# Performance work log

Hardware: AMD Instinct MI355X
Metric: run time of the kernel (lower is better)

## Reference

```python
import jax, jax.numpy as jnp
import numpy as np

SHIFT, REDUCE = 1, 2
B, L, E, H = 128, 64, 512, 512
T = 2 * L - 1  # valid binary-parse transition sequence length


def _make_transitions(rng):
    # Random *valid* shift-reduce sequences: L shifts, L-1 reduces, stack ends at 1.
    trans = np.zeros((B, T), dtype=np.int32)
    for b in range(B):
        stack, buf = 0, L
        for t in range(T):
            ops_left = T - t
            can_shift = buf > 0 and stack < ops_left
            can_reduce = stack >= 2
            if can_shift and can_reduce:
                act = SHIFT if rng.random() < 0.5 else REDUCE
            elif can_shift:
                act = SHIFT
            else:
                act = REDUCE
            if act == SHIFT:
                buf -= 1; stack += 1
            else:
                stack -= 1
            trans[b, t] = act
    return trans


def setup_inputs() -> dict:
    key = jax.random.key(0)
    k1, k2, k3, k4 = jax.random.split(key, 4)
    sentence = jax.random.normal(k1, (B, L, E), dtype=jnp.float32)
    transitions = jnp.asarray(_make_transitions(np.random.default_rng(0)))
    W_word = jax.random.normal(k2, (E, 2 * H), dtype=jnp.float32) / np.sqrt(E).astype(np.float32)
    b_word = jnp.zeros((2 * H,), dtype=jnp.float32)
    W_left = jax.random.normal(k3, (H, 5 * H), dtype=jnp.float32) / np.sqrt(H).astype(np.float32)
    W_right = jax.random.normal(k4, (H, 5 * H), dtype=jnp.float32) / np.sqrt(H).astype(np.float32)
    b_reduce = jnp.zeros((5 * H,), dtype=jnp.float32)
    return {"sentence": sentence, "transitions": transitions, "W_word": W_word,
            "b_word": b_word, "W_left": W_left, "W_right": W_right, "b_reduce": b_reduce}


def reference(sentence, transitions, W_word, b_word, W_left, W_right, b_reduce):
    Bx, Lx, _ = sentence.shape
    Hx = W_left.shape[0]
    Tx = transitions.shape[1]
    # word projection (no_batch_norm=True, dropout=0 in this config)
    out = sentence @ W_word + b_word                      # [B, L, 2H]
    h_buf, c_buf = jnp.split(out, 2, axis=2)              # buffers, popped front-to-back
    rows = jnp.arange(Bx)
    ops_left_seq = jnp.arange(Tx, 0, -1, dtype=jnp.int32)
    init = (jnp.zeros((Bx, Lx, Hx), out.dtype),           # stack h
            jnp.zeros((Bx, Lx, Hx), out.dtype),           # stack c
            jnp.zeros((Bx,), jnp.int32),                  # stack ptr
            jnp.zeros((Bx,), jnp.int32))                  # buffer ptr

    def step(carry, xs):
        sh, sc, sp, bp = carry
        act, ops = xs
        act = jnp.where(sp > ops, REDUCE, act)            # forced reduce (discrete stack)
        is_red = act == REDUCE
        is_shf = act == SHIFT
        r_idx = jnp.clip(sp - 1, 0, Lx - 1)
        l_idx = jnp.clip(sp - 2, 0, Lx - 1)
        hl, cl = sh[rows, l_idx], sc[rows, l_idx]
        hr, cr = sh[rows, r_idx], sc[rows, r_idx]
        # TreeLSTM Reduce cell
        gates = hl @ W_left + hr @ W_right + b_reduce     # [B, 5H]
        g, i, f1, f2, o = jnp.split(gates, 5, axis=1)
        c_red = jnp.tanh(g) * jax.nn.sigmoid(i) + jax.nn.sigmoid(f1) * cl + jax.nn.sigmoid(f2) * cr
        h_red = jax.nn.sigmoid(o) * jnp.tanh(c_red)
        b_idx = jnp.clip(bp, 0, Lx - 1)
        h_shf, c_shf = h_buf[rows, b_idx], c_buf[rows, b_idx]
        w_idx = jnp.where(is_red, l_idx, jnp.clip(sp, 0, Lx - 1))
        h_cur, c_cur = sh[rows, w_idx], sc[rows, w_idx]
        m_red, m_shf = is_red[:, None], is_shf[:, None]
        wh = jnp.where(m_red, h_red, jnp.where(m_shf, h_shf, h_cur))
        wc = jnp.where(m_red, c_red, jnp.where(m_shf, c_shf, c_cur))
        sh = sh.at[rows, w_idx].set(wh)
        sc = sc.at[rows, w_idx].set(wc)
        sp = sp + is_shf.astype(jnp.int32) - is_red.astype(jnp.int32)
        bp = bp + is_shf.astype(jnp.int32)
        return (sh, sc, sp, bp), None

    (sh, sc, sp, bp), _ = jax.lax.scan(step, init, (transitions.T, ops_left_seq))
    return sh[rows, jnp.clip(sp - 1, 0, Lx - 1)]          # [B, H] top of each stack
```

## Files before the change

### kernel.cpp

```cpp
#include <hip/hip_runtime.h>
#include <hip/hip_bf16.h>


#define Bn 128
#define Ln 64
#define En 512
#define Hn 512
#define Tn 127
#define LEAF_ROWS (Bn*Ln)
#define NODE_ROWS (Bn*(Ln-1))
#define TOT_ROWS (LEAF_ROWS+NODE_ROWS)
#define NLVL 64
#define NXCD 8
#define CAPX 512
#define NBLK 512
#define FPAD 16
#define MAXRANK 96
#define SPIN_CAP (1<<22)
#define GATE_STRIDE (512*1024)
#define WLDS_BYTES 65536
#define PART_BYTES (4*2*16*20*4)
#define DYN_BYTES (WLDS_BYTES + PART_BYTES)

#define OFF_CENSUS 0
#define OFF_RANK   (OFF_CENSUS + NXCD*FPAD)
#define OFF_SFLAG  (OFF_RANK + NBLK*FPAD)
#define OFF_SGEN   (OFF_SFLAG + NBLK*FPAD)
#define OFF_FX     (OFF_SGEN + FPAD)
#define OFF_GX     (OFF_FX + NXCD*MAXRANK*FPAD)
#define BAR_INTS   (OFF_GX + NXCD*FPAD)

typedef __attribute__((ext_vector_type(8))) short bf16x8;
typedef __attribute__((ext_vector_type(4))) float f32x4;

static __device__ __forceinline__ float bf2f(unsigned short u){
  unsigned v = ((unsigned)u) << 16;
  float f; __builtin_memcpy(&f, &v, 4); return f;
}
static __device__ __forceinline__ unsigned short f2bf(float f){
  unsigned u; __builtin_memcpy(&u, &f, 4);
  u = u + 0x7FFFu + ((u >> 16) & 1u);
  return (unsigned short)(u >> 16);
}
static __device__ __forceinline__ float sigm(float x){
  return 1.0f / (1.0f + __expf(-x));
}
static __device__ __forceinline__ float tanh_fast(float x){
  x = fminf(fmaxf(x, -15.0f), 15.0f);
  float t = __expf(2.0f * x);
  return (t - 1.0f) / (t + 1.0f);
}
static __device__ __forceinline__ int xcc_id(){
  unsigned v;
  asm volatile("s_getreg_b32 %0, hwreg(HW_REG_XCC_ID)" : "=s"(v));
  return (int)(v & 7);
}

static __device__ __forceinline__ void xcd_barrier(int* bar, int x, int rank, int nx, int epoch){
  __syncthreads();
  int* fx = bar + OFF_FX + x * MAXRANK * FPAD;
  int* gx = bar + OFF_GX + x * FPAD;
  int nxl = min(nx, MAXRANK);
  if (rank == 0){
    for (int i = threadIdx.x + 1; i < nxl; i += 256){
      int c = 0;
      while (__hip_atomic_load(&fx[i * FPAD], __ATOMIC_RELAXED, __HIP_MEMORY_SCOPE_AGENT) < epoch && c < SPIN_CAP){
        __builtin_amdgcn_s_sleep(1); ++c;
      }
    }
    __syncthreads();
    if (threadIdx.x == 0)
      __hip_atomic_store(gx, epoch, __ATOMIC_RELAXED, __HIP_MEMORY_SCOPE_AGENT);
  } else {
    if (threadIdx.x == 0){
      __hip_atomic_store(&fx[rank * FPAD], epoch, __ATOMIC_RELAXED, __HIP_MEMORY_SCOPE_AGENT);
      int c = 0;
      while (__hip_atomic_load(gx, __ATOMIC_RELAXED, __HIP_MEMORY_SCOPE_AGENT) < epoch && c < SPIN_CAP){
        __builtin_amdgcn_s_sleep(2); ++c;
      }
    }
    __syncthreads();
  }
  asm volatile("" ::: "memory");
}


__global__ void cvt_vec4(const float4* __restrict__ x, ushort4* __restrict__ y, int n4){
  int i = blockIdx.x * 256 + threadIdx.x;
  if (i < n4){
    float4 v = x[i];
    ushort4 o;
    o.x = f2bf(v.x); o.y = f2bf(v.y); o.z = f2bf(v.z); o.w = f2bf(v.w);
    y[i] = o;
  }
}

__global__ void transpose_cvt(const float* __restrict__ src, unsigned short* __restrict__ dstT,
                              int CS, int DS, int koff){
  __shared__ float tile[32][33];
  int c0 = blockIdx.x * 32, r0 = blockIdx.y * 32;
  int tx = threadIdx.x, ty = threadIdx.y;
  for (int i = ty; i < 32; i += 8) tile[i][tx] = src[(size_t)(r0 + i) * CS + c0 + tx];
  __syncthreads();
  for (int i = ty; i < 32; i += 8)
    dstT[(size_t)(c0 + i) * DS + koff + r0 + tx] = f2bf(tile[tx][i]);
}

__global__ void precompute_ctrl(const int* __restrict__ trans,
                                int* __restrict__ srcL, int* __restrict__ srcR,
                                int* __restrict__ dstv, int* __restrict__ cnt,
                                int* __restrict__ outsrc, int* __restrict__ bar){
  __shared__ int stk[Bn][Ln + 1];
  __shared__ int scnt[NXCD * NLVL];
  __shared__ int smaxl[NXCD];
  int b = threadIdx.x;
  for (int i = b; i < NXCD * NLVL; i += 128) scnt[i] = 0;
  if (b < NXCD) smaxl[b] = 0;
  for (int i = b; i < BAR_INTS; i += 128) bar[i] = 0;
  __syncthreads();
  int x = b & 7;
  int sp = 0, bp = 0, nodecnt = 0;
  int act_next = trans[b * Tn];
  for (int t = 0; t < Tn; t++){
    int act = act_next;
    if (t + 1 < Tn) act_next = trans[b * Tn + t + 1];
    int ops = Tn - t;
    if (sp > ops) act = 2;
    if (act == 2){
      int R = stk[b][sp - 1], L = stk[b][sp - 2];
      int lvl = max(R >> 20, L >> 20) + 1;
      int slot = atomicAdd(&scnt[x * NLVL + lvl], 1);
      int base = (x * NLVL + lvl) * CAPX + slot;
      srcL[base] = (L & 0xFFFFF) * Hn;
      srcR[base] = (R & 0xFFFFF) * Hn;
      int noderow = LEAF_ROWS + b * (Ln - 1) + nodecnt;
      dstv[base] = noderow * Hn;
      stk[b][sp - 2] = noderow | (lvl << 20);
      sp -= 1; nodecnt++;
    } else {
      stk[b][sp] = b * Ln + min(bp, Ln - 1);
      sp += 1; bp += 1;
    }
  }
  int root = stk[b][max(sp - 1, 0)];
  outsrc[b] = (root & 0xFFFFF) * Hn;
  atomicMax(&smaxl[x], root >> 20);
  __syncthreads();
  for (int i = b; i < NXCD * NLVL; i += 128) cnt[i] = scnt[i];
  if (b < NXCD) cnt[NXCD * NLVL + b] = smaxl[b];
}

__global__ __launch_bounds__(256) void word_gemm(
    const unsigned short* __restrict__ SB, const unsigned short* __restrict__ WwT,
    const float* __restrict__ b_word,
    unsigned short* __restrict__ HB, float* __restrict__ CF){
  int mt = blockIdx.x;
  int nt = blockIdx.y;
  int tid = threadIdx.x, w = tid >> 6, lane = tid & 63;
  int wm = w >> 1, wn = w & 1;
  int rc = lane & 15, lg = lane >> 4;
  const unsigned short* ap0 = SB + (size_t)(mt * 64 + wm * 32 + rc) * En + lg * 8;
  const unsigned short* ap1 = ap0 + (size_t)16 * En;
  const unsigned short* bp0 = WwT + (size_t)(nt * 128 + wn * 64 + rc) * En + lg * 8;
  f32x4 acc[2][4];
  #pragma unroll
  for (int h = 0; h < 2; h++)
    #pragma unroll
    for (int nb = 0; nb < 4; nb++) acc[h][nb] = (f32x4){0.f,0.f,0.f,0.f};

  bf16x8 a0c = *(const bf16x8*)ap0;
  bf16x8 a1c = *(const bf16x8*)ap1;
  bf16x8 bc[4];
  #pragma unroll
  for (int nb = 0; nb < 4; nb++) bc[nb] = *(const bf16x8*)(bp0 + (size_t)nb * 16 * En);

  #pragma unroll
  for (int j = 0; j < 16; ++j){
    bf16x8 a0n, a1n, bn[4];
    if (j < 15){
      int kn = (j + 1) * 32;
      a0n = *(const bf16x8*)(ap0 + kn);
      a1n = *(const bf16x8*)(ap1 + kn);
      #pragma unroll
      for (int nb = 0; nb < 4; nb++)
        bn[nb] = *(const bf16x8*)(bp0 + (size_t)nb * 16 * En + kn);
    }
    #pragma unroll
    for (int nb = 0; nb < 4; nb++){
      acc[0][nb] = __builtin_amdgcn_mfma_f32_16x16x32_bf16(a0c, bc[nb], acc[0][nb], 0, 0, 0);
      acc[1][nb] = __builtin_amdgcn_mfma_f32_16x16x32_bf16(a1c, bc[nb], acc[1][nb], 0, 0, 0);
    }
    a0c = a0n; a1c = a1n;
    #pragma unroll
    for (int nb = 0; nb < 4; nb++) bc[nb] = bn[nb];
  }
  #pragma unroll
  for (int nb = 0; nb < 4; nb++){
    int col = nt * 128 + wn * 64 + nb * 16 + rc;
    float bw = b_word[col];
    #pragma unroll
    for (int h = 0; h < 2; h++){
      #pragma unroll
      for (int q = 0; q < 4; q++){
        int row = mt * 64 + wm * 32 + h * 16 + lg * 4 + q;
        float v = acc[h][nb][q] + bw;
        if (col < Hn) HB[(size_t)row * Hn + col] = f2bf(v);
        else          CF[(size_t)row * Hn + (col - Hn)] = v;
      }
    }
  }
}

template<bool LDSB>
static __device__ __forceinline__ void tile64(
    int u0, int t, int nr, const int* __restrict__ sL, const int* __restrict__ sR,
    const int* __restrict__ dl,
    unsigned short* __restrict__ HB, float* __restrict__ CF,
    const unsigned short* __restrict__ WT, const float* __restrict__ b_red,
    const unsigned short* __restrict__ wlds, int rc, int lg)
{
  int base = t * 64;
  int offL[4], offR[4];
  #pragma unroll
  for (int m = 0; m < 4; m++){
    int i = min(base + m * 16 + rc, nr - 1);
    offL[m] = sL[i]; offR[m] = sR[i];
  }
  f32x4 acc[5][4];
  #pragma unroll
  for (int g = 0; g < 5; g++)
    #pragma unroll
    for (int m = 0; m < 4; m++) acc[g][m] = (f32x4){0.f,0.f,0.f,0.f};

  int bswz = (rc & 7) << 3;
  const unsigned short* gb = WT + (size_t)(u0 + rc) * 1024 + lg * 8;

  bf16x8 a_cur[4], b_cur[3];
  #pragma unroll
  for (int m = 0; m < 4; m++) a_cur[m] = *(const bf16x8*)(HB + offL[m] + lg * 8);
  #pragma unroll
  for (int g = 0; g < 3; g++)
    b_cur[g] = *(const bf16x8*)(gb + (size_t)(g + 2) * GATE_STRIDE);

  #pragma unroll 4
  for (int j = 0; j < 32; ++j){
    bf16x8 a_nxt[4], b_nxt[3];
    if (j < 31){
      int kn = (j + 1) * 32 + lg * 8;
      #pragma unroll
      for (int m = 0; m < 4; m++){
        const unsigned short* ap = (j + 1 < 16) ? (HB + offL[m] + kn) : (HB + offR[m] + (kn - 512));
        a_nxt[m] = *(const bf16x8*)ap;
      }
      #pragma unroll
      for (int g = 0; g < 3; g++)
        b_nxt[g] = *(const bf16x8*)(gb + (size_t)(g + 2) * GATE_STRIDE + (j + 1) * 32);
    }
    int k = j * 32 + lg * 8;
    #pragma unroll
    for (int g = 0; g < 2; g++){
      bf16x8 bb;
      if (LDSB) bb = *(const bf16x8*)&wlds[(size_t)(g * 16 + rc) * 1024 + (k ^ bswz)];
      else      bb = *(const bf16x8*)(gb + (size_t)g * GATE_STRIDE + j * 32);
      #pragma unroll
      for (int m = 0; m < 4; m++)
        acc[g][m] = __builtin_amdgcn_mfma_f32_16x16x32_bf16(a_cur[m], bb, acc[g][m], 0, 0, 0);
    }
    #pragma unroll
    for (int g = 0; g < 3; g++){
      #pragma unroll
      for (int m = 0; m < 4; m++)
        acc[g + 2][m] = __builtin_amdgcn_mfma_f32_16x16x32_bf16(a_cur[m], b_cur[g], acc[g + 2][m], 0, 0, 0);
    }
    #pragma unroll
    for (int m = 0; m < 4; m++) a_cur[m] = a_nxt[m];
    #pragma unroll
    for (int g = 0; g < 3; g++) b_cur[g] = b_nxt[g];
  }
  int colu = u0 + rc;
  float bs[5];
  #pragma unroll
  for (int g = 0; g < 5; g++) bs[g] = b_red[g * Hn + colu];
  #pragma unroll
  for (int m = 0; m < 4; m++){
    #pragma unroll
    for (int q = 0; q < 4; q++){
      int i = base + m * 16 + lg * 4 + q;
      if (i < nr){
        int oL = sL[i], oR = sR[i], oD = dl[i];
        float gv = tanh_fast(acc[0][m][q] + bs[0]);
        float iv = sigm(acc[1][m][q] + bs[1]);
        float f1 = sigm(acc[2][m][q] + bs[2]);
        float f2 = sigm(acc[3][m][q] + bs[3]);
        float ov = sigm(acc[4][m][q] + bs[4]);
        float cl = __builtin_nontemporal_load(CF + oL + colu);
        float cr = __builtin_nontemporal_load(CF + oR + colu);
        float cv = gv * iv + f1 * cl + f2 * cr;
        float hv = ov * tanh_fast(cv);
        __builtin_nontemporal_store(cv, CF + oD + colu);
        HB[oD + colu] = f2bf(hv);
      }
    }
  }
}

static __device__ __forceinline__ void tile16(
    int u0, int t, int nr, const int* __restrict__ sL, const int* __restrict__ sR,
    const int* __restrict__ dl,
    unsigned short* __restrict__ HB, float* __restrict__ CF,
    const unsigned short* __restrict__ WT, const float* __restrict__ b_red,
    const unsigned short* __restrict__ wlds, float (*part)[2][16][20],
    int tid, int w, int rc, int lg)
{
  int base = t * 16;
  int er = tid >> 4, eu = tid & 15;
  int i0 = min(base + rc, nr - 1);
  int offA = (w >= 2) ? sR[i0] : sL[i0];
  int ie = min(base + er, nr - 1);
  int oL = sL[ie], oR = sR[ie], oD = dl[ie];
  int colu = u0 + eu;
  float cl = __builtin_nontemporal_load(CF + oL + colu);
  float cr = __builtin_nontemporal_load(CF + oR + colu);

  int k0 = w * 256;
  int abase = (w >= 2) ? (k0 - 512) : k0;
  const unsigned short* ap = HB + offA + abase + lg * 8;
  int bswz = (rc & 7) << 3;
  const unsigned short* gb = WT + (size_t)(u0 + rc) * 1024;

  f32x4 acc[5];
  #pragma unroll
  for (int g = 0; g < 5; g++) acc[g] = (f32x4){0.f,0.f,0.f,0.f};

  bf16x8 a_cur = *(const bf16x8*)ap;
  bf16x8 b_cur[3];
  #pragma unroll
  for (int g = 0; g < 3; g++)
    b_cur[g] = *(const bf16x8*)(gb + (size_t)(g + 2) * GATE_STRIDE + k0 + lg * 8);

  #pragma unroll
  for (int j = 0; j < 8; ++j){
    bf16x8 a_nxt, b_nxt[3];
    if (j < 7){
      a_nxt = *(const bf16x8*)(ap + (j + 1) * 32);
      #pragma unroll
      for (int g = 0; g < 3; g++)
        b_nxt[g] = *(const bf16x8*)(gb + (size_t)(g + 2) * GATE_STRIDE + k0 + (j + 1) * 32 + lg * 8);
    }
    int k = k0 + j * 32 + lg * 8;
    #pragma unroll
    for (int g = 0; g < 2; g++){
      bf16x8 bb = *(const bf16x8*)&wlds[(size_t)(g * 16 + rc) * 1024 + (k ^ bswz)];
      acc[g] = __builtin_amdgcn_mfma_f32_16x16x32_bf16(a_cur, bb, acc[g], 0, 0, 0);
    }
    #pragma unroll
    for (int g = 0; g < 3; g++)
      acc[g + 2] = __builtin_amdgcn_mfma_f32_16x16x32_bf16(a_cur, b_cur[g], acc[g + 2], 0, 0, 0);
    a_cur = a_nxt;
    #pragma unroll
    for (int g = 0; g < 3; g++) b_cur[g] = b_nxt[g];
  }
  float sg[5];
  #pragma unroll
  for (int r = 0; r < 3; ++r){
    int ng = (r < 2) ? 2 : 1;
    #pragma unroll
    for (int gi = 0; gi < 2; ++gi){
      if (gi < ng){
        int g = r * 2 + gi;
        #pragma unroll
        for (int q = 0; q < 4; q++) part[w][gi][lg * 4 + q][rc] = acc[g][q];
      }
    }
    __syncthreads();
    #pragma unroll
    for (int gi = 0; gi < 2; ++gi){
      if (gi < ng)
        sg[r * 2 + gi] = part[0][gi][er][eu] + part[1][gi][er][eu]
                       + part[2][gi][er][eu] + part[3][gi][er][eu];
    }
    __syncthreads();
  }
  int i = base + er;
  if (i < nr){
    float gv = tanh_fast(sg[0] + b_red[colu]);
    float iv = sigm(sg[1] + b_red[Hn + colu]);
    float f1 = sigm(sg[2] + b_red[2 * Hn + colu]);
    float f2 = sigm(sg[3] + b_red[3 * Hn + colu]);
    float ov = sigm(sg[4] + b_red[4 * Hn + colu]);
    float cv = gv * iv + f1 * cl + f2 * cr;
    float hv = ov * tanh_fast(cv);
    __builtin_nontemporal_store(cv, CF + oD + colu);
    HB[oD + colu] = f2bf(hv);
  }
  __syncthreads();
}

extern __shared__ char dynbuf[];

__global__ __launch_bounds__(256, 2) void tree_kernel(
    unsigned short* __restrict__ HB, float* __restrict__ CF,
    const unsigned short* __restrict__ WT, const float* __restrict__ b_red,
    const int* __restrict__ srcL, const int* __restrict__ srcR,
    const int* __restrict__ dstv, const int* __restrict__ cnt,
    const int* __restrict__ outsrc, float* __restrict__ out, int* bar){
  unsigned short* wlds = (unsigned short*)dynbuf;
  float (*part)[2][16][20] = (float(*)[2][16][20])(dynbuf + WLDS_BYTES);
  int bid = blockIdx.x;
  int tid = threadIdx.x, w = tid >> 6, lane = tid & 63;
  int rc = lane & 15, lg = lane >> 4;

  int x = xcc_id();
  if (tid == 0){
    int r = __hip_atomic_fetch_add(&bar[OFF_CENSUS + x * FPAD], 1,
                                   __ATOMIC_RELAXED, __HIP_MEMORY_SCOPE_AGENT);
    __hip_atomic_store(&bar[OFF_RANK + bid * FPAD], r, __ATOMIC_RELAXED, __HIP_MEMORY_SCOPE_AGENT);
  }
  __syncthreads();
  int rank = min(__hip_atomic_load(&bar[OFF_RANK + bid * FPAD], __ATOMIC_RELAXED, __HIP_MEMORY_SCOPE_AGENT),
                 MAXRANK - 1);
  int ub = rank & 31;
  int u0 = ub * 16;

  for (int gg = tid; gg < 4096; gg += 256){
    int row = gg >> 7;
    int k = (gg & 127) * 8;
    int u = row & 15, g = row >> 4;
    bf16x8 v = *(const bf16x8*)(WT + (size_t)(g * 512 + u0 + u) * 1024 + k);
    int kx = k ^ ((u & 7) << 3);
    *(bf16x8*)&wlds[(size_t)row * 1024 + kx] = v;
  }
  __syncthreads();

  {
    int* sfl  = bar + OFF_SFLAG;
    int* sgen = bar + OFF_SGEN;
    if (bid == 0){
      for (int i = tid; i < NBLK; i += 256){
        if (i){
          int c = 0;
          while (__hip_atomic_load(&sfl[i * FPAD], __ATOMIC_RELAXED, __HIP_MEMORY_SCOPE_AGENT) == 0 && c < SPIN_CAP){
            __builtin_amdgcn_s_sleep(1); ++c;
          }
        }
      }
      __syncthreads();
      if (tid == 0) __hip_atomic_store(sgen, 1, __ATOMIC_RELAXED, __HIP_MEMORY_SCOPE_AGENT);
    } else {
      if (tid == 0){
        __hip_atomic_store(&sfl[bid * FPAD], 1, __ATOMIC_RELAXED, __HIP_MEMORY_SCOPE_AGENT);
        int c = 0;
        while (__hip_atomic_load(sgen, __ATOMIC_RELAXED, __HIP_MEMORY_SCOPE_AGENT) == 0 && c < SPIN_CAP){
          __builtin_amdgcn_s_sleep(2); ++c;
        }
      }
      __syncthreads();
    }
  }
  int nx = max(__hip_atomic_load(&bar[OFF_CENSUS + x * FPAD], __ATOMIC_RELAXED, __HIP_MEMORY_SCOPE_AGENT), 1);

  int maxlvl = cnt[NXCD * NLVL + x];
  int epoch = 1;
  for (int lvl = 1; lvl <= maxlvl; ++lvl, ++epoch){
    int nr = cnt[x * NLVL + lvl];
    const int* sL = srcL + (x * NLVL + lvl) * CAPX;
    const int* sR = srcR + (x * NLVL + lvl) * CAPX;
    const int* dl = dstv + (x * NLVL + lvl) * CAPX;
    if (nr > 0){
      if (nx >= 32){
        int nstr = (nx - 1 - ub) / 32 + 1;
        int stripe = rank >> 5;
        if (nr >= 128){
          int ntl = (nr + 63) >> 6;
          for (int t = stripe * 4 + w; t < ntl; t += nstr * 4)
            tile64<true>(u0, t, nr, sL, sR, dl, HB, CF, WT, b_red, wlds, rc, lg);
        } else {
          int ntl16 = (nr + 15) >> 4;
          for (int t = stripe; t < ntl16; t += nstr)
            tile16(u0, t, nr, sL, sR, dl, HB, CF, WT, b_red, wlds, part, tid, w, rc, lg);
        }
      } else {
        int ntl = (nr + 63) >> 6;
        int nwv = nx * 4, wid = rank * 4 + w;
        int ntask = ntl * 32;
        for (int task = wid; task < ntask; task += nwv)
          tile64<false>((task / ntl) * 16, task % ntl, nr, sL, sR, dl, HB, CF, WT, b_red, wlds, rc, lg);
      }
    }
    xcd_barrier(bar, x, rank, nx, epoch);
  }

  for (int j = rank; j < 16; j += min(nx, MAXRANK)){
    int b = x + 8 * j;
    int src = outsrc[b];
    out[b * Hn + tid]       = bf2f(HB[src + tid]);
    out[b * Hn + tid + 256] = bf2f(HB[src + tid + 256]);
  }
}

extern "C" void kernel_launch(void* const* d_in, const int* in_sizes, int n_in,
                              void* d_out, int out_size, void* d_ws, size_t ws_size,
                              hipStream_t stream){
  (void)in_sizes; (void)n_in; (void)out_size; (void)ws_size;
  const float* sentence = (const float*)d_in[0];
  const int*   trans    = (const int*)d_in[1];
  const float* W_word   = (const float*)d_in[2];
  const float* b_word   = (const float*)d_in[3];
  const float* W_left   = (const float*)d_in[4];
  const float* W_right  = (const float*)d_in[5];
  const float* b_red    = (const float*)d_in[6];

  char* ws = (char*)d_ws;
  size_t off = 0;
  auto alloc = [&](size_t bytes) -> void* {
    void* p = ws + off;
    off += (bytes + 255) & ~((size_t)255);
    return p;
  };
  unsigned short* HB  = (unsigned short*)alloc((size_t)TOT_ROWS * Hn * 2);
  float*          CF  = (float*)alloc((size_t)TOT_ROWS * Hn * 4);
  unsigned short* WT  = (unsigned short*)alloc((size_t)2560 * 1024 * 2);
  unsigned short* SB  = (unsigned short*)alloc((size_t)LEAF_ROWS * En * 2);
  unsigned short* WwT = (unsigned short*)alloc((size_t)1024 * En * 2);
  int* srcL   = (int*)alloc((size_t)NXCD * NLVL * CAPX * 4);
  int* srcR   = (int*)alloc((size_t)NXCD * NLVL * CAPX * 4);
  int* dstv   = (int*)alloc((size_t)NXCD * NLVL * CAPX * 4);
  int* cnt    = (int*)alloc((size_t)(NXCD * NLVL + NXCD) * 4);
  int* outsrc = (int*)alloc((size_t)Bn * 4);
  int* bar    = (int*)alloc((size_t)BAR_INTS * 4);
  float* outp = (float*)d_out;

  hipFuncSetAttribute(reinterpret_cast<const void*>(tree_kernel),
                      hipFuncAttributeMaxDynamicSharedMemorySize, DYN_BYTES);

  cvt_vec4<<<(LEAF_ROWS * En / 4) / 256, 256, 0, stream>>>((const float4*)sentence, (ushort4*)SB, LEAF_ROWS * En / 4);
  transpose_cvt<<<dim3(1024 / 32, En / 32), dim3(32, 8), 0, stream>>>(W_word, WwT, 1024, En, 0);
  transpose_cvt<<<dim3(2560 / 32, Hn / 32), dim3(32, 8), 0, stream>>>(W_left, WT, 2560, 1024, 0);
  transpose_cvt<<<dim3(2560 / 32, Hn / 32), dim3(32, 8), 0, stream>>>(W_right, WT, 2560, 1024, 512);
  precompute_ctrl<<<1, 128, 0, stream>>>(trans, srcL, srcR, dstv, cnt, outsrc, bar);
  word_gemm<<<dim3(128, 8), 256, 0, stream>>>(SB, WwT, b_word, HB, CF);
  tree_kernel<<<NBLK, 256, DYN_BYTES, stream>>>(HB, CF, WT, b_red, srcL, srcR, dstv, cnt, outsrc, outp, bar);
}
```

Baseline: 609.0 us.

## Deepen word GEMM prefetch, swap grid order, defer tree-cell c loads

The word projection GEMM now prefetches two K-steps ahead using a three-slot register ring instead of one. Its grid is transposed so consecutive blocks share the same A rows across N tiles, which should improve L2 reuse of the sentence tiles. In the tree reduce tile, the cl/cr cell-state loads and index lookups move from before the MFMA loop to the epilogue, cutting register pressure during the main loop. The catch is that their latency is no longer hidden behind the matmul.

New measurement: 598.2 us, median of 2. Within noise of the previous version (-1.8%).

```diff
diff --git a/kernel.cpp b/kernel.cpp
--- a/kernel.cpp
+++ b/kernel.cpp
@@ -154,8 +154,8 @@
     const unsigned short* __restrict__ SB, const unsigned short* __restrict__ WwT,
     const float* __restrict__ b_word,
     unsigned short* __restrict__ HB, float* __restrict__ CF){
-  int mt = blockIdx.x;
-  int nt = blockIdx.y;
+  int nt = blockIdx.x;
+  int mt = blockIdx.y;
   int tid = threadIdx.x, w = tid >> 6, lane = tid & 63;
   int wm = w >> 1, wn = w & 1;
   int rc = lane & 15, lg = lane >> 4;
@@ -168,31 +168,31 @@
     #pragma unroll
     for (int nb = 0; nb < 4; nb++) acc[h][nb] = (f32x4){0.f,0.f,0.f,0.f};
 
-  bf16x8 a0c = *(const bf16x8*)ap0;
-  bf16x8 a1c = *(const bf16x8*)ap1;
-  bf16x8 bc[4];
-  #pragma unroll
-  for (int nb = 0; nb < 4; nb++) bc[nb] = *(const bf16x8*)(bp0 + (size_t)nb * 16 * En);
-
+  bf16x8 aS0[3], aS1[3], bS[4][3];
+  #pragma unroll
+  for (int s = 0; s < 2; s++){
+    aS0[s] = *(const bf16x8*)(ap0 + s * 32);
+    aS1[s] = *(const bf16x8*)(ap1 + s * 32);
+    #pragma unroll
+    for (int nb = 0; nb < 4; nb++)
+      bS[nb][s] = *(const bf16x8*)(bp0 + (size_t)nb * 16 * En + s * 32);
+  }
   #pragma unroll
   for (int j = 0; j < 16; ++j){
-    bf16x8 a0n, a1n, bn[4];
-    if (j < 15){
-      int kn = (j + 1) * 32;
-      a0n = *(const bf16x8*)(ap0 + kn);
-      a1n = *(const bf16x8*)(ap1 + kn);
+    const int cur = j % 3, n2 = (j + 2) % 3;
+    if (j < 14){
+      int kn = (j + 2) * 32;
+      aS0[n2] = *(const bf16x8*)(ap0 + kn);
+      aS1[n2] = *(const bf16x8*)(ap1 + kn);
       #pragma unroll
       for (int nb = 0; nb < 4; nb++)
-        bn[nb] = *(const bf16x8*)(bp0 + (size_t)nb * 16 * En + kn);
+        bS[nb][n2] = *(const bf16x8*)(bp0 + (size_t)nb * 16 * En + kn);
     }
     #pragma unroll
     for (int nb = 0; nb < 4; nb++){
-      acc[0][nb] = __builtin_amdgcn_mfma_f32_16x16x32_bf16(a0c, bc[nb], acc[0][nb], 0, 0, 0);
-      acc[1][nb] = __builtin_amdgcn_mfma_f32_16x16x32_bf16(a1c, bc[nb], acc[1][nb], 0, 0, 0);
-    }
-    a0c = a0n; a1c = a1n;
-    #pragma unroll
-    for (int nb = 0; nb < 4; nb++) bc[nb] = bn[nb];
+      acc[0][nb] = __builtin_amdgcn_mfma_f32_16x16x32_bf16(aS0[cur], bS[nb][cur], acc[0][nb], 0, 0, 0);
+      acc[1][nb] = __builtin_amdgcn_mfma_f32_16x16x32_bf16(aS1[cur], bS[nb][cur], acc[1][nb], 0, 0, 0);
+    }
   }
   #pragma unroll
   for (int nb = 0; nb < 4; nb++){
@@ -313,15 +313,8 @@
     int tid, int w, int rc, int lg)
 {
   int base = t * 16;
-  int er = tid >> 4, eu = tid & 15;
   int i0 = min(base + rc, nr - 1);
   int offA = (w >= 2) ? sR[i0] : sL[i0];
-  int ie = min(base + er, nr - 1);
-  int oL = sL[ie], oR = sR[ie], oD = dl[ie];
-  int colu = u0 + eu;
-  float cl = __builtin_nontemporal_load(CF + oL + colu);
-  float cr = __builtin_nontemporal_load(CF + oR + colu);
-
   int k0 = w * 256;
   int abase = (w >= 2) ? (k0 - 512) : k0;
   const unsigned short* ap = HB + offA + abase + lg * 8;
@@ -360,6 +353,7 @@
     #pragma unroll
     for (int g = 0; g < 3; g++) b_cur[g] = b_nxt[g];
   }
+  int er = tid >> 4, eu = tid & 15;
   float sg[5];
   #pragma unroll
   for (int r = 0; r < 3; ++r){
@@ -383,11 +377,15 @@
   }
   int i = base + er;
   if (i < nr){
+    int colu = u0 + eu;
+    int oL = sL[i], oR = sR[i], oD = dl[i];
     float gv = tanh_fast(sg[0] + b_red[colu]);
     float iv = sigm(sg[1] + b_red[Hn + colu]);
     float f1 = sigm(sg[2] + b_red[2 * Hn + colu]);
     float f2 = sigm(sg[3] + b_red[3 * Hn + colu]);
     float ov = sigm(sg[4] + b_red[4 * Hn + colu]);
+    float cl = __builtin_nontemporal_load(CF + oL + colu);
+    float cr = __builtin_nontemporal_load(CF + oR + colu);
     float cv = gv * iv + f1 * cl + f2 * cr;
     float hv = ov * tanh_fast(cv);
     __builtin_nontemporal_store(cv, CF + oD + colu);
@@ -538,6 +536,6 @@
   transpose_cvt<<<dim3(2560 / 32, Hn / 32), dim3(32, 8), 0, stream>>>(W_left, WT, 2560, 1024, 0);
   transpose_cvt<<<dim3(2560 / 32, Hn / 32), dim3(32, 8), 0, stream>>>(W_right, WT, 2560, 1024, 512);
   precompute_ctrl<<<1, 128, 0, stream>>>(trans, srcL, srcR, dstv, cnt, outsrc, bar);
-  word_gemm<<<dim3(128, 8), 256, 0, stream>>>(SB, WwT, b_word, HB, CF);
+  word_gemm<<<dim3(8, LEAF_ROWS / 64), 256, 0, stream>>>(SB, WwT, b_word, HB, CF);
   tree_kernel<<<NBLK, 256, DYN_BYTES, stream>>>(HB, CF, WT, b_red, srcL, srcR, dstv, cnt, outsrc, outp, bar);
 }
```
